# Kernel optimization log

Hardware: AMD Instinct MI355X
Metric: run time of the kernel (lower is better)

Reference implementation:

```python
import jax, jax.numpy as jnp
import numpy as np


def _2div(arr):
    arr_res = arr.copy()
    arr_pieces = []
    pa = 0
    st = 0
    needdivcnt = 0
    for i, a in enumerate(arr):
        if a != pa:
            arr_pieces.append([st, i])
            if i - st != 1:
                needdivcnt += 1
            pa = a
            st = i
    arr_pieces.append([st, len(arr)])
    if len(arr) - st != 1:
        needdivcnt += 1
    offset = range(len(arr_pieces), len(arr_pieces) + needdivcnt)
    p = 0
    for arr_p in arr_pieces:
        length = arr_p[1] - arr_p[0]
        if length == 1:
            continue
        half_len = int(np.ceil(length / 2))
        for j in range(arr_p[0] + half_len, arr_p[1]):
            arr_res[j] = offset[p]
        p += 1
    return arr_res


def get_division_tree(n_agents):
    agent2divitreeindex = np.arange(n_agents)
    np.random.shuffle(agent2divitreeindex)
    max_div = np.ceil(np.log2(n_agents)).astype(int)
    levels = np.zeros(shape=(max_div + 1, n_agents), dtype=int)
    for ith in range(1, len(levels)):
        levels[ith, :] = _2div(levels[ith - 1, :])
    res_levels = levels.copy()
    for i, idx in enumerate(agent2divitreeindex):
        res_levels[:, i] = levels[:, idx]
    return res_levels


def setup_inputs() -> dict:
    B, A, H, NACT = 2048, 50, 512, 64
    F = H + A  # in-features of first Linear (hidden + one-hot agent id)
    np.random.seed(0)
    div_tree = get_division_tree(A)
    routing = jnp.asarray(div_tree[-1], dtype=jnp.int32)  # max_level routing: agent -> net index
    key = jax.random.key(0)
    k0, k1, k2 = jax.random.split(key, 3)
    x_in = jax.random.normal(k0, (B, A, H), dtype=jnp.float32)
    # stacked per-net parameters (n_nets == n_agent independent 2-layer MLPs)
    W1 = jax.random.normal(k1, (A, F, H), dtype=jnp.float32) * (1.0 / np.sqrt(F))
    b1 = jnp.zeros((A, H), dtype=jnp.float32)
    W2 = jax.random.normal(k2, (A, H, NACT), dtype=jnp.float32) * (1.0 / np.sqrt(H))
    b2 = jnp.zeros((A, NACT), dtype=jnp.float32)
    return {"x_in": x_in, "W1": W1, "b1": b1, "W2": W2, "b2": b2, "routing": routing}


def reference(x_in, W1, b1, W2, b2, routing):
    # x_in: [B, A, H]; routing: [A] int (which net each agent uses)
    B, A, H = x_in.shape
    # add_onehot_id_at_last_dim: append agent-id one-hot -> [B, A, H+A]
    onehot = jnp.broadcast_to(jnp.eye(A, dtype=x_in.dtype), (B, A, A))
    x0 = jnp.concatenate([x_in, onehot], axis=-1)
    # gather routed expert weights per agent
    W1r, b1r = W1[routing], b1[routing]   # [A, H+A, H], [A, H]
    W2r, b2r = W2[routing], b2[routing]   # [A, H, NACT], [A, NACT]
    h = jax.nn.relu(jnp.einsum('baf,afh->bah', x0, W1r) + b1r)
    out = jnp.einsum('bah,ahn->ban', h, W2r) + b2r  # [B, A, NACT]
    return out
```

## Files before the change

### kernel.cpp

```cpp
#include <hip/hip_runtime.h>

typedef __attribute__((ext_vector_type(8))) short bf16x8;
typedef __attribute__((ext_vector_type(4))) float f32x4;
typedef __attribute__((ext_vector_type(4))) unsigned short u16x4;
typedef __attribute__((ext_vector_type(8))) unsigned short u16x8;

#define B_ 2048
#define A_ 50
#define H_ 512
#define NACT_ 64
#define F_ 562
#define BM_ 64
#define BK_ 32
#define NSTEP_ (H_ / BK_)
#define AH_ (A_ * H_)

#define WS_W1T 0
#define WS_W2T ((size_t)A_ * H_ * H_ * 2)
#define WS_B1 (WS_W2T + (size_t)A_ * NACT_ * H_ * 2)
#define WS_B2 (WS_B1 + (size_t)A_ * H_ * 4)

static __device__ __forceinline__ unsigned short f2bf(float f) {
  unsigned int u = __builtin_bit_cast(unsigned int, f);
  u += 0x7fffu + ((u >> 16) & 1u);
  return (unsigned short)(u >> 16);
}

static __device__ __forceinline__ void gld_lds16(const unsigned short* src,
                                                 unsigned short* dst) {
  __builtin_amdgcn_global_load_lds(
      (const __attribute__((address_space(1))) unsigned int*)(const void*)src,
      (__attribute__((address_space(3))) unsigned int*)(void*)dst, 16, 0, 0);
}

static __device__ __forceinline__ int clamp_r(int r) {
  return r < 0 ? 0 : (r > A_ - 1 ? A_ - 1 : r);
}

__global__ void prep_w1(const float* __restrict__ w1,
                        const int* __restrict__ routing,
                        unsigned short* __restrict__ w1t) {
  const int bid = blockIdx.x;
  const int a = bid / 64;
  const int tile = bid - a * 64;
  const int tk = tile & 7, tj = tile >> 3;
  const int k0 = tk * 64, j0 = tj * 64;
  const int r = clamp_r(routing[a]);
  __shared__ float tl[64][65];
  const int t = threadIdx.x;
  const int c = t & 63, q = t >> 6;
#pragma unroll
  for (int i = 0; i < 16; ++i) {
    const int kl = q + i * 4;
    tl[kl][c] = w1[((size_t)r * F_ + k0 + kl) * H_ + j0 + c];
  }
  __syncthreads();
#pragma unroll
  for (int it = 0; it < 2; ++it) {
    const int item = it * 256 + t;
    const int jl = item >> 3, kc = item & 7;
    const int j = j0 + jl;
    const int ts = (k0 + kc * 8) >> 5;
    u16x8 v;
#pragma unroll
    for (int e = 0; e < 8; ++e) v[e] = f2bf(tl[kc * 8 + e][jl]);
    unsigned short* dst = w1t + (((size_t)a * 16 + ts) * H_ + j) * 32 +
                          (size_t)(((kc & 3) ^ (j & 3)) << 3);
    *(u16x8*)dst = v;
  }
}

__global__ void prep_w2(const float* __restrict__ w2,
                        const int* __restrict__ routing,
                        unsigned short* __restrict__ w2t) {
  const int bid = blockIdx.x;
  const int a = bid >> 3;
  const int tk = bid & 7;
  const int k0 = tk * 64;
  const int r = clamp_r(routing[a]);
  __shared__ float tl[64][65];
  const int t = threadIdx.x;
  const int c = t & 63, q = t >> 6;
#pragma unroll
  for (int i = 0; i < 16; ++i) {
    const int kl = q + i * 4;
    tl[kl][c] = w2[((size_t)r * H_ + k0 + kl) * NACT_ + c];
  }
  __syncthreads();
#pragma unroll
  for (int i = 0; i < 16; ++i) {
    const int nl = q + i * 4;
    w2t[((size_t)a * NACT_ + nl) * H_ + k0 + c] = f2bf(tl[c][nl]);
  }
}

__global__ void prep_bias(const float* __restrict__ w1,
                          const float* __restrict__ b1,
                          const float* __restrict__ b2,
                          const int* __restrict__ routing,
                          float* __restrict__ bias1, float* __restrict__ bias2) {
  const int a = blockIdx.x;
  const int t = threadIdx.x;
  const int r = clamp_r(routing[a]);
  bias1[a * H_ + t] = b1[(size_t)r * H_ + t] + w1[((size_t)r * F_ + H_ + a) * H_ + t];
  if (t < NACT_) bias2[a * NACT_ + t] = b2[r * NACT_ + t];
}

__global__ __launch_bounds__(512, 2) void divtree_main(
    const float* __restrict__ x, const unsigned short* __restrict__ w1t,
    const unsigned short* __restrict__ w2t, const float* __restrict__ bias1,
    const float* __restrict__ bias2, float* __restrict__ out) {
  __shared__ union {
    struct {
      unsigned short w1[2][H_ * BK_];
      unsigned short xs[2][BM_ * BK_];
    } st;
    unsigned short h[BM_ * H_];
    float outb[BM_][66];
  } sm;

  const int bid = blockIdx.x;
  const int swz = (bid & 7) * 200 + (bid >> 3);
  const int a = swz >> 5;
  const int mblk = swz & 31;
  const int b0 = mblk * BM_;

  const int tid = threadIdx.x;
  const int lane = tid & 63;
  const int w = tid >> 6;
  const int l16 = lane & 15;
  const int lk = lane >> 4;
  const int sxor = lk ^ (l16 & 3);

  const int wj = w * 64;

  const unsigned short* w1ta = w1t + (size_t)a * (H_ * H_);

  const int r2 = lane >> 5;
  const int cc = lane & 31;
  const int xq = cc & 7;
  const int xact = cc >> 3;
  const float* xpt =
      x + ((size_t)(b0 + (w << 3) + r2) * A_ + (size_t)a) * H_ + (size_t)cc * 4;
  int xs_off[4];
#pragma unroll
  for (int i = 0; i < 4; ++i) {
    const int row = (w << 3) + 2 * i + r2;
    xs_off[i] = row * BK_ + ((xq >> 1) ^ (row & 3)) * 8 + (xq & 1) * 4;
  }

  const int afr_base = (wj + l16) * BK_ + sxor * 8;
  const int bfr_base = l16 * BK_ + sxor * 8;

  f32x4 acc[4][4];
#pragma unroll
  for (int i = 0; i < 4; ++i)
#pragma unroll
    for (int j = 0; j < 4; ++j) acc[i][j] = (f32x4){0.f, 0.f, 0.f, 0.f};

  f32x4 xr[4];
  u16x4 xbf[4];

  {
#pragma unroll
    for (int i = 0; i < 4; ++i)
      xr[i] = *(const f32x4*)(xpt + (size_t)(2 * i) * AH_);
#pragma unroll
    for (int i = 0; i < 4; ++i)
      gld_lds16(w1ta + ((size_t)(i * 512 + tid) << 3),
                sm.st.w1[0] + (size_t)(i * 512 + (w << 6)) * 8);
#pragma unroll
    for (int i = 0; i < 4; ++i)
#pragma unroll
      for (int e = 0; e < 4; ++e) xbf[i][e] = f2bf(xr[i][e]);
    if (xact == 0) {
#pragma unroll
      for (int i = 0; i < 4; ++i) *(u16x4*)(sm.st.xs[0] + xs_off[i]) = xbf[i];
    }
  }
  __syncthreads();

#pragma unroll
  for (int t = 0; t < NSTEP_; ++t) {
    const int buf = t & 1;
    const bool pf = (t + 1 < NSTEP_);
    if (((t & 3) == 3) && pf) {
      const float* p = xpt + (size_t)(t + 1) * BK_;
#pragma unroll
      for (int i = 0; i < 4; ++i)
        xr[i] = *(const f32x4*)(p + (size_t)(2 * i) * AH_);
    }
    if (pf) {
      const unsigned short* wsrc = w1ta + (size_t)(t + 1) * (H_ * BK_);
#pragma unroll
      for (int i = 0; i < 4; ++i)
        gld_lds16(wsrc + ((size_t)(i * 512 + tid) << 3),
                  sm.st.w1[buf ^ 1] + (size_t)(i * 512 + (w << 6)) * 8);
    }
    {
      const unsigned short* w1s = sm.st.w1[buf];
      const unsigned short* xss = sm.st.xs[buf];
      bf16x8 bfr[4];
#pragma unroll
      for (int mf = 0; mf < 4; ++mf)
        bfr[mf] = *(const bf16x8*)(xss + bfr_base + mf * (16 * BK_));
#pragma unroll
      for (int jf = 0; jf < 4; ++jf) {
        const bf16x8 afr = *(const bf16x8*)(w1s + afr_base + jf * (16 * BK_));
#pragma unroll
        for (int mf = 0; mf < 4; ++mf)
          acc[jf][mf] = __builtin_amdgcn_mfma_f32_16x16x32_bf16(
              afr, bfr[mf], acc[jf][mf], 0, 0, 0);
      }
    }
    if (((t & 3) == 3) && pf) {
#pragma unroll
      for (int i = 0; i < 4; ++i)
#pragma unroll
        for (int e = 0; e < 4; ++e) xbf[i][e] = f2bf(xr[i][e]);
    }
    if (pf && xact == ((t + 1) & 3)) {
#pragma unroll
      for (int i = 0; i < 4; ++i)
        *(u16x4*)(sm.st.xs[buf ^ 1] + xs_off[i]) = xbf[i];
    }
    __syncthreads();
  }

  const float* b1p = bias1 + a * H_;
#pragma unroll
  for (int jf = 0; jf < 4; ++jf) {
    const f32x4 bv = *(const f32x4*)(b1p + wj + jf * 16 + lk * 4);
    const int cbase = (wj >> 3) + jf * 2 + (lk >> 1);
    const int half4 = (lk & 1) * 4;
#pragma unroll
    for (int mf = 0; mf < 4; ++mf) {
      u16x4 hv;
#pragma unroll
      for (int r = 0; r < 4; ++r) {
        float f = acc[jf][mf][r] + bv[r];
        f = f > 0.f ? f : 0.f;
        hv[r] = f2bf(f);
      }
      const int m = mf * 16 + l16;
      const int off = m * H_ + ((cbase ^ (l16 & 7))) * 8 + half4;
      *(u16x4*)(sm.h + off) = hv;
    }
  }
  __syncthreads();

  const int m0 = (w & 1) * 32;
  const int n0 = (w >> 1) * 16;
  const unsigned short* w2p =
      w2t + ((size_t)a * NACT_ + n0 + l16) * H_ + lk * 8;
  f32x4 acc2[2];
  acc2[0] = (f32x4){0.f, 0.f, 0.f, 0.f};
  acc2[1] = (f32x4){0.f, 0.f, 0.f, 0.f};
#pragma unroll
  for (int kf = 0; kf < 16; ++kf) {
    const bf16x8 bf2 = *(const bf16x8*)(w2p + kf * 32);
#pragma unroll
    for (int mf = 0; mf < 2; ++mf) {
      const int row = m0 + mf * 16 + l16;
      const int off = row * H_ + (((kf * 4 + lk) ^ (l16 & 7))) * 8;
      const bf16x8 af2 = *(const bf16x8*)(sm.h + off);
      acc2[mf] = __builtin_amdgcn_mfma_f32_16x16x32_bf16(af2, bf2, acc2[mf],
                                                         0, 0, 0);
    }
  }
  const float b2v = bias2[a * NACT_ + n0 + l16];
  __syncthreads();
#pragma unroll
  for (int mf = 0; mf < 2; ++mf)
#pragma unroll
    for (int r = 0; r < 4; ++r)
      sm.outb[m0 + mf * 16 + lk * 4 + r][n0 + l16] = acc2[mf][r] + b2v;
  __syncthreads();

  {
    const int row = tid >> 3;
    const int q8 = (tid & 7) * 8;
    const f32x4 v0 = *(const f32x4*)(&sm.outb[row][q8]);
    const f32x4 v1 = *(const f32x4*)(&sm.outb[row][q8 + 4]);
    float* op = out + ((size_t)(b0 + row) * A_ + a) * NACT_ + q8;
    *(f32x4*)op = v0;
    *(f32x4*)(op + 4) = v1;
  }
}

extern "C" void kernel_launch(void* const* d_in, const int* in_sizes, int n_in,
                              void* d_out, int out_size, void* d_ws,
                              size_t ws_size, hipStream_t stream) {
  const float* x = (const float*)d_in[0];
  const float* w1 = (const float*)d_in[1];
  const float* b1 = (const float*)d_in[2];
  const float* w2 = (const float*)d_in[3];
  const float* b2 = (const float*)d_in[4];
  const int* routing = (const int*)d_in[5];
  float* out = (float*)d_out;

  char* ws = (char*)d_ws;
  unsigned short* w1t = (unsigned short*)(ws + WS_W1T);
  unsigned short* w2t = (unsigned short*)(ws + WS_W2T);
  float* bias1 = (float*)(ws + WS_B1);
  float* bias2 = (float*)(ws + WS_B2);

  prep_w1<<<A_ * 64, 256, 0, stream>>>(w1, routing, w1t);
  prep_w2<<<A_ * 8, 256, 0, stream>>>(w2, routing, w2t);
  prep_bias<<<A_, 512, 0, stream>>>(w1, b1, b2, routing, bias1, bias2);
  divtree_main<<<A_ * (B_ / BM_), 512, 0, stream>>>(x, w1t, w2t, bias1, bias2,
                                                    out);
}
```

Before: 177.1 us.

## Rework layer-1 pipeline with per-step x loads, manual waitcnt barriers and priority

Each thread now loads one float4 of x per K-step, prefetched three steps ahead in a rotating register buffer, instead of batched loads every four steps by a subset of lanes. The main loop swaps __syncthreads for explicit s_waitcnt plus s_barrier at the top of each step, and raises wave priority around the MFMA block. It also simplifies the w1 prep store indexing and asks for 4 blocks per CU in launch bounds. The aim is smoother memory latency hiding and more resident waves, at the cost of register pressure under the tighter bound and fragile hand-written vmcnt accounting.

```diff
diff --git a/kernel.cpp b/kernel.cpp
--- a/kernel.cpp
+++ b/kernel.cpp
@@ -13,7 +13,6 @@
 #define BM_ 64
 #define BK_ 32
 #define NSTEP_ (H_ / BK_)
-#define AH_ (A_ * H_)
 
 #define WS_W1T 0
 #define WS_W2T ((size_t)A_ * H_ * H_ * 2)
@@ -57,15 +56,13 @@
   __syncthreads();
 #pragma unroll
   for (int it = 0; it < 2; ++it) {
-    const int item = it * 256 + t;
-    const int jl = item >> 3, kc = item & 7;
-    const int j = j0 + jl;
-    const int ts = (k0 + kc * 8) >> 5;
+    const int jl = t >> 2, c2 = t & 3;
+    const int kc = it * 4 + (c2 ^ (jl & 3));
     u16x8 v;
 #pragma unroll
     for (int e = 0; e < 8; ++e) v[e] = f2bf(tl[kc * 8 + e][jl]);
-    unsigned short* dst = w1t + (((size_t)a * 16 + ts) * H_ + j) * 32 +
-                          (size_t)(((kc & 3) ^ (j & 3)) << 3);
+    unsigned short* dst = w1t +
+        (((size_t)a * 16 + tk * 2 + it) * H_ + j0 + jl) * 32 + c2 * 8;
     *(u16x8*)dst = v;
   }
 }
@@ -106,7 +103,7 @@
   if (t < NACT_) bias2[a * NACT_ + t] = b2[r * NACT_ + t];
 }
 
-__global__ __launch_bounds__(512, 2) void divtree_main(
+__global__ __launch_bounds__(512, 4) void divtree_main(
     const float* __restrict__ x, const unsigned short* __restrict__ w1t,
     const unsigned short* __restrict__ w2t, const float* __restrict__ bias1,
     const float* __restrict__ bias2, float* __restrict__ out) {
@@ -136,18 +133,11 @@
 
   const unsigned short* w1ta = w1t + (size_t)a * (H_ * H_);
 
-  const int r2 = lane >> 5;
-  const int cc = lane & 31;
-  const int xq = cc & 7;
-  const int xact = cc >> 3;
-  const float* xpt =
-      x + ((size_t)(b0 + (w << 3) + r2) * A_ + (size_t)a) * H_ + (size_t)cc * 4;
-  int xs_off[4];
-#pragma unroll
-  for (int i = 0; i < 4; ++i) {
-    const int row = (w << 3) + 2 * i + r2;
-    xs_off[i] = row * BK_ + ((xq >> 1) ^ (row & 3)) * 8 + (xq & 1) * 4;
-  }
+  const int xrow = tid >> 3;
+  const int xq = tid & 7;
+  const float* xbase =
+      x + ((size_t)(b0 + xrow) * A_ + (size_t)a) * H_ + (size_t)xq * 4;
+  const int xs_off = xrow * BK_ + ((xq >> 1) ^ (xrow & 3)) * 8 + (xq & 1) * 4;
 
   const int afr_base = (wj + l16) * BK_ + sxor * 8;
   const int bfr_base = l16 * BK_ + sxor * 8;
@@ -158,74 +148,67 @@
 #pragma unroll
     for (int j = 0; j < 4; ++j) acc[i][j] = (f32x4){0.f, 0.f, 0.f, 0.f};
 
-  f32x4 xr[4];
-  u16x4 xbf[4];
+  f32x4 xr[3];
 
   {
-#pragma unroll
-    for (int i = 0; i < 4; ++i)
-      xr[i] = *(const f32x4*)(xpt + (size_t)(2 * i) * AH_);
+    const f32x4 xv0 = *(const f32x4*)xbase;
 #pragma unroll
     for (int i = 0; i < 4; ++i)
       gld_lds16(w1ta + ((size_t)(i * 512 + tid) << 3),
                 sm.st.w1[0] + (size_t)(i * 512 + (w << 6)) * 8);
-#pragma unroll
-    for (int i = 0; i < 4; ++i)
-#pragma unroll
-      for (int e = 0; e < 4; ++e) xbf[i][e] = f2bf(xr[i][e]);
-    if (xact == 0) {
-#pragma unroll
-      for (int i = 0; i < 4; ++i) *(u16x4*)(sm.st.xs[0] + xs_off[i]) = xbf[i];
-    }
-  }
-  __syncthreads();
+    xr[1] = *(const f32x4*)(xbase + 1 * BK_);
+    xr[2] = *(const f32x4*)(xbase + 2 * BK_);
+    u16x4 v;
+#pragma unroll
+    for (int e = 0; e < 4; ++e) v[e] = f2bf(xv0[e]);
+    *(u16x4*)(sm.st.xs[0] + xs_off) = v;
+  }
 
 #pragma unroll
   for (int t = 0; t < NSTEP_; ++t) {
     const int buf = t & 1;
-    const bool pf = (t + 1 < NSTEP_);
-    if (((t & 3) == 3) && pf) {
-      const float* p = xpt + (size_t)(t + 1) * BK_;
-#pragma unroll
-      for (int i = 0; i < 4; ++i)
-        xr[i] = *(const f32x4*)(p + (size_t)(2 * i) * AH_);
-    }
-    if (pf) {
+    if (t <= NSTEP_ - 3)
+      asm volatile("s_waitcnt vmcnt(1) lgkmcnt(0)" ::: "memory");
+    else
+      asm volatile("s_waitcnt vmcnt(0) lgkmcnt(0)" ::: "memory");
+    __builtin_amdgcn_sched_barrier(0);
+    __builtin_amdgcn_s_barrier();
+    __builtin_amdgcn_sched_barrier(0);
+    if (t + 1 < NSTEP_) {
       const unsigned short* wsrc = w1ta + (size_t)(t + 1) * (H_ * BK_);
+      unsigned short* wdst = sm.st.w1[buf ^ 1];
 #pragma unroll
       for (int i = 0; i < 4; ++i)
         gld_lds16(wsrc + ((size_t)(i * 512 + tid) << 3),
-                  sm.st.w1[buf ^ 1] + (size_t)(i * 512 + (w << 6)) * 8);
-    }
-    {
-      const unsigned short* w1s = sm.st.w1[buf];
-      const unsigned short* xss = sm.st.xs[buf];
-      bf16x8 bfr[4];
+                  wdst + (size_t)(i * 512 + (w << 6)) * 8);
+    }
+    if (t + 3 < NSTEP_)
+      xr[(t + 3) % 3] = *(const f32x4*)(xbase + (size_t)(t + 3) * BK_);
+    const unsigned short* w1s = sm.st.w1[buf];
+    const unsigned short* xss = sm.st.xs[buf];
+    bf16x8 bfr[4];
+#pragma unroll
+    for (int mf = 0; mf < 4; ++mf)
+      bfr[mf] = *(const bf16x8*)(xss + bfr_base + mf * (16 * BK_));
+    __builtin_amdgcn_s_setprio(1);
+#pragma unroll
+    for (int jf = 0; jf < 4; ++jf) {
+      const bf16x8 afr = *(const bf16x8*)(w1s + afr_base + jf * (16 * BK_));
 #pragma unroll
       for (int mf = 0; mf < 4; ++mf)
-        bfr[mf] = *(const bf16x8*)(xss + bfr_base + mf * (16 * BK_));
-#pragma unroll
-      for (int jf = 0; jf < 4; ++jf) {
-        const bf16x8 afr = *(const bf16x8*)(w1s + afr_base + jf * (16 * BK_));
-#pragma unroll
-        for (int mf = 0; mf < 4; ++mf)
-          acc[jf][mf] = __builtin_amdgcn_mfma_f32_16x16x32_bf16(
-              afr, bfr[mf], acc[jf][mf], 0, 0, 0);
-      }
-    }
-    if (((t & 3) == 3) && pf) {
-#pragma unroll
-      for (int i = 0; i < 4; ++i)
-#pragma unroll
-        for (int e = 0; e < 4; ++e) xbf[i][e] = f2bf(xr[i][e]);
-    }
-    if (pf && xact == ((t + 1) & 3)) {
-#pragma unroll
-      for (int i = 0; i < 4; ++i)
-        *(u16x4*)(sm.st.xs[buf ^ 1] + xs_off[i]) = xbf[i];
-    }
-    __syncthreads();
-  }
+        acc[jf][mf] = __builtin_amdgcn_mfma_f32_16x16x32_bf16(
+            afr, bfr[mf], acc[jf][mf], 0, 0, 0);
+    }
+    __builtin_amdgcn_s_setprio(0);
+    if (t + 1 < NSTEP_) {
+      const f32x4 xv = xr[(t + 1) % 3];
+      u16x4 v;
+#pragma unroll
+      for (int e = 0; e < 4; ++e) v[e] = f2bf(xv[e]);
+      *(u16x4*)(sm.st.xs[buf ^ 1] + xs_off) = v;
+    }
+  }
+  __syncthreads();
 
   const float* b1p = bias1 + a * H_;
 #pragma unroll
```

Result: faster. 143.2 us (-19.2%).
